# Kernel optimization log

Measured on AMD Instinct MI355X. Metric: run time of the kernel, lower is better.

## Reference

```python
import jax, jax.numpy as jnp
import numpy as np

N, C, H, W = 4, 128, 28, 28
K, D = 64, 512  # num_clusters, dim_center
EPS = 1e-12     # torch F.normalize eps


def setup_inputs() -> dict:
    key = jax.random.key(0)
    k1, k2, k3, k4 = jax.random.split(key, 4)
    x = jax.random.normal(k1, (N, C, H, W), dtype=jnp.float32)
    # 1x1 conv weight (dim_center, dim) with kaiming-normal fan_out scale, bias zero
    conv_w = jax.random.normal(k2, (D, C), dtype=jnp.float32) * np.float32(np.sqrt(2.0 / D))
    conv_b = jnp.zeros((D,), dtype=jnp.float32)
    # centroids initialized with torch.rand -> uniform [0,1)
    centroids = jax.random.uniform(k3, (K, D), dtype=jnp.float32)
    return {"x": x, "conv_w": conv_w, "conv_b": conv_b, "centroids": centroids}


def reference(x, conv_w, conv_b, centroids):
    n, c, h, w = x.shape
    # descriptor-wise L2 normalization over channel dim (torch F.normalize, p=2, dim=1)
    nrm = jnp.sqrt(jnp.sum(x * x, axis=1, keepdims=True))
    xn = x / jnp.maximum(nrm, EPS)
    # 1x1 conv == per-pixel matmul: (N,C,H,W) x (D,C) -> (N,D,H,W)
    feat = jnp.einsum('nchw,dc->ndhw', xn, conv_w) + conv_b[None, :, None, None]
    xf = feat.reshape(n, D, h * w)  # (N, D, P)
    # residual[n,k,d,p] = xf[n,d,p] - centroids[k,d]
    resid = xf[:, None, :, :] - centroids[None, :, :, None]  # (N, K, D, P)
    soft_assign = jax.nn.softmax(resid, axis=-1)             # softmax over spatial P
    vlad = jnp.sum(soft_assign * xf[:, None, :, :], axis=-1)  # (N, K, D)
    return vlad
```

## Files before the change

### kernel.cpp

```cpp
#include <hip/hip_runtime.h>
#include <math.h>

#define NB 4
#define CC 128
#define HW 784
#define KK 64
#define DD 512
#define TD 8
#define BLK 832
#define UNR 16

__global__ __launch_bounds__(BLK) void netvlad_fused_kernel(
    const float* __restrict__ x, const float* __restrict__ w,
    const float* __restrict__ b, float* __restrict__ out)
{
    __shared__ float w_s[CC][TD];
    __shared__ float feat_s[TD][HW];
    __shared__ float g_s[TD];

    const int tid = threadIdx.x;
    const int n  = blockIdx.x >> 6;
    const int d0 = (blockIdx.x & 63) * TD;
    const bool act = tid < HW;

    for (int i = tid; i < CC * TD; i += BLK) {
        int c = i >> 3, j = i & 7;
        w_s[c][j] = w[(size_t)(d0 + j) * CC + c];
    }
    __syncthreads();

    if (act) {
        const float* xp = x + (size_t)n * CC * HW + tid;
        float acc[TD];
        #pragma unroll
        for (int j = 0; j < TD; ++j) acc[j] = 0.f;
        float sq = 0.f;

        for (int cc = 0; cc < CC; cc += UNR) {
            float xv[UNR];
            #pragma unroll
            for (int u = 0; u < UNR; ++u)
                xv[u] = xp[(size_t)(cc + u) * HW];
            #pragma unroll
            for (int u = 0; u < UNR; ++u) {
                const int c = cc + u;
                float4 wlo = *(const float4*)&w_s[c][0];
                float4 whi = *(const float4*)&w_s[c][4];
                float xvu = xv[u];
                sq = fmaf(xvu, xvu, sq);
                acc[0] = fmaf(wlo.x, xvu, acc[0]);
                acc[1] = fmaf(wlo.y, xvu, acc[1]);
                acc[2] = fmaf(wlo.z, xvu, acc[2]);
                acc[3] = fmaf(wlo.w, xvu, acc[3]);
                acc[4] = fmaf(whi.x, xvu, acc[4]);
                acc[5] = fmaf(whi.y, xvu, acc[5]);
                acc[6] = fmaf(whi.z, xvu, acc[6]);
                acc[7] = fmaf(whi.w, xvu, acc[7]);
            }
        }

        float r = 1.0f / fmaxf(sqrtf(sq), 1e-12f);
        #pragma unroll
        for (int j = 0; j < TD; ++j)
            feat_s[j][tid] = fmaf(acc[j], r, b[d0 + j]);
    }
    __syncthreads();

    const int lane = tid & 63;
    const int wave = tid >> 6;
    if (wave < TD) {
        const int j = wave;
        float m = -INFINITY;
        for (int q = lane; q < HW; q += 64) m = fmaxf(m, feat_s[j][q]);
        #pragma unroll
        for (int off = 32; off; off >>= 1) m = fmaxf(m, __shfl_xor(m, off, 64));
        float s = 0.f, ws = 0.f;
        for (int q = lane; q < HW; q += 64) {
            float f = feat_s[j][q];
            float e = __expf(f - m);
            s += e;
            ws = fmaf(e, f, ws);
        }
        #pragma unroll
        for (int off = 32; off; off >>= 1) {
            s  += __shfl_xor(s, off, 64);
            ws += __shfl_xor(ws, off, 64);
        }
        if (lane == 0) g_s[j] = ws / s;
    }
    __syncthreads();

    if (tid < KK * TD) {
        int k = tid >> 3, j = tid & 7;
        out[(size_t)n * KK * DD + (size_t)k * DD + d0 + j] = g_s[j];
    }
}

extern "C" void kernel_launch(void* const* d_in, const int* in_sizes, int n_in,
                              void* d_out, int out_size, void* d_ws, size_t ws_size,
                              hipStream_t stream) {
    const float* x = (const float*)d_in[0];
    const float* w = (const float*)d_in[1];
    const float* b = (const float*)d_in[2];
    float* out = (float*)d_out;

    netvlad_fused_kernel<<<NB * (DD / TD), BLK, 0, stream>>>(x, w, b, out);
}
```

Measured before the change: 17.57 us.

## Split spatial dimension across blocks with partial softmax sums and finalize kernel

```diff
diff --git a/kernel.cpp b/kernel.cpp
--- a/kernel.cpp
+++ b/kernel.cpp
@@ -7,21 +7,24 @@
 #define KK 64
 #define DD 512
 #define TD 8
-#define BLK 832
-#define UNR 16
+#define SLICES 8
+#define SPX 98
+#define BLK 128
 
-__global__ __launch_bounds__(BLK) void netvlad_fused_kernel(
+__global__ __launch_bounds__(BLK) void netvlad_gemm_partial(
     const float* __restrict__ x, const float* __restrict__ w,
-    const float* __restrict__ b, float* __restrict__ out)
+    const float* __restrict__ b, float2* __restrict__ pws)
 {
     __shared__ float w_s[CC][TD];
-    __shared__ float feat_s[TD][HW];
-    __shared__ float g_s[TD];
+    __shared__ float2 red_s[2][TD];
 
     const int tid = threadIdx.x;
-    const int n  = blockIdx.x >> 6;
-    const int d0 = (blockIdx.x & 63) * TD;
-    const bool act = tid < HW;
+    const int bid = blockIdx.x;
+    const int n   = bid >> 9;
+    const int dg  = (bid >> 3) & 63;
+    const int sl  = bid & 7;
+    const int d0  = dg * TD;
+    const int p0  = sl * SPX;
 
     for (int i = tid; i < CC * TD; i += BLK) {
         int c = i >> 3, j = i & 7;
@@ -29,71 +32,84 @@
     }
     __syncthreads();
 
-    if (act) {
-        const float* xp = x + (size_t)n * CC * HW + tid;
-        float acc[TD];
+    const bool act = tid < SPX;
+    const int  p   = p0 + (act ? tid : (SPX - 1));
+    const float* xp = x + (size_t)n * CC * HW + p;
+
+    float acc[TD];
+    #pragma unroll
+    for (int j = 0; j < TD; ++j) acc[j] = 0.f;
+    float sq = 0.f;
+
+    for (int cc = 0; cc < CC; cc += 16) {
+        float xv[16];
         #pragma unroll
-        for (int j = 0; j < TD; ++j) acc[j] = 0.f;
-        float sq = 0.f;
+        for (int u = 0; u < 16; ++u)
+            xv[u] = xp[(size_t)(cc + u) * HW];
+        #pragma unroll
+        for (int u = 0; u < 16; ++u) {
+            const int c = cc + u;
+            float4 wlo = *(const float4*)&w_s[c][0];
+            float4 whi = *(const float4*)&w_s[c][4];
+            float xvu = xv[u];
+            sq = fmaf(xvu, xvu, sq);
+            acc[0] = fmaf(wlo.x, xvu, acc[0]);
+            acc[1] = fmaf(wlo.y, xvu, acc[1]);
+            acc[2] = fmaf(wlo.z, xvu, acc[2]);
+            acc[3] = fmaf(wlo.w, xvu, acc[3]);
+            acc[4] = fmaf(whi.x, xvu, acc[4]);
+            acc[5] = fmaf(whi.y, xvu, acc[5]);
+            acc[6] = fmaf(whi.z, xvu, acc[6]);
+            acc[7] = fmaf(whi.w, xvu, acc[7]);
+        }
+    }
 
-        for (int cc = 0; cc < CC; cc += UNR) {
-            float xv[UNR];
-            #pragma unroll
-            for (int u = 0; u < UNR; ++u)
-                xv[u] = xp[(size_t)(cc + u) * HW];
-            #pragma unroll
-            for (int u = 0; u < UNR; ++u) {
-                const int c = cc + u;
-                float4 wlo = *(const float4*)&w_s[c][0];
-                float4 whi = *(const float4*)&w_s[c][4];
-                float xvu = xv[u];
-                sq = fmaf(xvu, xvu, sq);
-                acc[0] = fmaf(wlo.x, xvu, acc[0]);
-                acc[1] = fmaf(wlo.y, xvu, acc[1]);
-                acc[2] = fmaf(wlo.z, xvu, acc[2]);
-                acc[3] = fmaf(wlo.w, xvu, acc[3]);
-                acc[4] = fmaf(whi.x, xvu, acc[4]);
-                acc[5] = fmaf(whi.y, xvu, acc[5]);
-                acc[6] = fmaf(whi.z, xvu, acc[6]);
-                acc[7] = fmaf(whi.w, xvu, acc[7]);
-            }
-        }
+    const float r = 1.0f / fmaxf(sqrtf(sq), 1e-12f);
+    float se[TD], we[TD];
+    #pragma unroll
+    for (int j = 0; j < TD; ++j) {
+        float f = fmaf(acc[j], r, b[d0 + j]);
+        float e = act ? __expf(f) : 0.f;
+        se[j] = e;
+        we[j] = act ? e * f : 0.f;
+    }
 
-        float r = 1.0f / fmaxf(sqrtf(sq), 1e-12f);
-        #pragma unroll
-        for (int j = 0; j < TD; ++j)
-            feat_s[j][tid] = fmaf(acc[j], r, b[d0 + j]);
-    }
-    __syncthreads();
-
-    const int lane = tid & 63;
-    const int wave = tid >> 6;
-    if (wave < TD) {
-        const int j = wave;
-        float m = -INFINITY;
-        for (int q = lane; q < HW; q += 64) m = fmaxf(m, feat_s[j][q]);
-        #pragma unroll
-        for (int off = 32; off; off >>= 1) m = fmaxf(m, __shfl_xor(m, off, 64));
-        float s = 0.f, ws = 0.f;
-        for (int q = lane; q < HW; q += 64) {
-            float f = feat_s[j][q];
-            float e = __expf(f - m);
-            s += e;
-            ws = fmaf(e, f, ws);
-        }
+    #pragma unroll
+    for (int j = 0; j < TD; ++j) {
         #pragma unroll
         for (int off = 32; off; off >>= 1) {
-            s  += __shfl_xor(s, off, 64);
-            ws += __shfl_xor(ws, off, 64);
+            se[j] += __shfl_xor(se[j], off, 64);
+            we[j] += __shfl_xor(we[j], off, 64);
         }
-        if (lane == 0) g_s[j] = ws / s;
     }
+    const int lane = tid & 63;
+    const int wv   = tid >> 6;
+    if (lane < TD) red_s[wv][lane] = make_float2(se[lane], we[lane]);
     __syncthreads();
+    if (tid < TD) {
+        float2 a = red_s[0][tid], c2 = red_s[1][tid];
+        pws[(size_t)(n * DD + d0 + tid) * SLICES + sl] =
+            make_float2(a.x + c2.x, a.y + c2.y);
+    }
+}
 
-    if (tid < KK * TD) {
-        int k = tid >> 3, j = tid & 7;
-        out[(size_t)n * KK * DD + (size_t)k * DD + d0 + j] = g_s[j];
+__global__ __launch_bounds__(512) void netvlad_finalize(
+    const float2* __restrict__ pws, float* __restrict__ out)
+{
+    const int d  = threadIdx.x;
+    const int n  = blockIdx.x >> 3;
+    const int ks = (blockIdx.x & 7) * 8;
+    float s = 0.f, ws = 0.f;
+    #pragma unroll
+    for (int i = 0; i < SLICES; ++i) {
+        float2 v = pws[(size_t)(n * DD + d) * SLICES + i];
+        s  += v.x;
+        ws += v.y;
     }
+    float g = ws / s;
+    #pragma unroll
+    for (int i = 0; i < 8; ++i)
+        out[(size_t)n * KK * DD + (size_t)(ks + i) * DD + d] = g;
 }
 
 extern "C" void kernel_launch(void* const* d_in, const int* in_sizes, int n_in,
@@ -102,7 +118,9 @@
     const float* x = (const float*)d_in[0];
     const float* w = (const float*)d_in[1];
     const float* b = (const float*)d_in[2];
-    float* out = (float*)d_out;
+    float2* pws = (float2*)d_ws;
+    float* out  = (float*)d_out;
 
-    netvlad_fused_kernel<<<NB * (DD / TD), BLK, 0, stream>>>(x, w, b, out);
+    netvlad_gemm_partial<<<NB * (DD / TD) * SLICES, BLK, 0, stream>>>(x, w, b, pws);
+    netvlad_finalize<<<32, 512, 0, stream>>>(pws, out);
 }
```

After: 22.98 us. 30.8% more time.
